# Optimization experiments

Hardware: AMD Instinct MI355X
Metric: run time of the kernel (lower is better)

## Reference

```python
import jax, jax.numpy as jnp
import numpy as np

B, H, W, C = 2, 128, 128, 256
D = 64          # attention_dim
NH = 1          # num_heads
P = 18          # num_random_points
N = H * W
EPS = 1e-5


def _layernorm(x, gamma, beta):
    mu = jnp.mean(x, axis=-1, keepdims=True)
    var = jnp.var(x, axis=-1, keepdims=True)
    return (x - mu) * jax.lax.rsqrt(var + EPS) * gamma + beta


def setup_inputs() -> dict:
    key = jax.random.key(0)
    ks = jax.random.split(key, 12)
    s = 0.02
    inp = {
        "X": jax.random.normal(ks[0], (B, H, W, C), dtype=jnp.float32),
        "selected_indices": jax.random.randint(ks[1], (B, N, P), 0, N),
        "topk": 1,
        "pos_enc": jax.random.normal(ks[2], (1, H, W, C), dtype=jnp.float32),
        "Wq": jax.random.normal(ks[3], (C, NH * D), dtype=jnp.float32) * s,
        "bq": jnp.zeros((NH * D,), dtype=jnp.float32),
        "Wk": jax.random.normal(ks[4], (C, NH * D), dtype=jnp.float32) * s,
        "bk": jnp.zeros((NH * D,), dtype=jnp.float32),
        "Wv": jax.random.normal(ks[5], (C, NH * D), dtype=jnp.float32) * s,
        "bv": jnp.zeros((NH * D,), dtype=jnp.float32),
        "Wo": jax.random.normal(ks[6], (NH * D, C), dtype=jnp.float32) * s,
        "bo": jnp.zeros((C,), dtype=jnp.float32),
        "W1": jax.random.normal(ks[7], (C, 4 * C), dtype=jnp.float32) * s,
        "b1": jnp.zeros((4 * C,), dtype=jnp.float32),
        "W2": jax.random.normal(ks[8], (4 * C, C), dtype=jnp.float32) * s,
        "b2": jnp.zeros((C,), dtype=jnp.float32),
        "g1": jnp.ones((C,), dtype=jnp.float32),
        "be1": jnp.zeros((C,), dtype=jnp.float32),
        "g2": jnp.ones((C,), dtype=jnp.float32),
        "be2": jnp.zeros((C,), dtype=jnp.float32),
    }
    return inp


def reference(X, selected_indices, topk, pos_enc, Wq, bq, Wk, bk, Wv, bv,
              Wo, bo, W1, b1, W2, b2, g1, be1, g2, be2):
    # forward_wotopk path (topk == 1)
    Xp = X + pos_enc                                  # [B,H,W,C]
    Q = (Xp @ Wq + bq).reshape(B, N, NH, D)
    K = (Xp @ Wk + bk).reshape(B, N, NH, D)
    V = (Xp @ Wv + bv).reshape(B, N, NH, D)

    # gather 18 random K/V rows per query pixel: [B,N,P,NH,D]
    gather = jax.vmap(lambda kv, idx: kv[idx])        # per-batch fancy index
    Ksel = gather(K, selected_indices)
    Vsel = gather(V, selected_indices)

    scores = jnp.einsum('bihd,bijhd->bijh', Q, Ksel) / jnp.sqrt(
        jnp.asarray(D, dtype=jnp.float32))
    attn = jax.nn.softmax(scores, axis=2)             # softmax over the P points
    ctx = jnp.einsum('bijh,bijhd->bihd', attn, Vsel).reshape(B, N, NH * D)

    out = (ctx @ Wo + bo).reshape(B, H, W, C)
    Xn = _layernorm(Xp + out, g1, be1)
    ffn = jax.nn.relu(Xn @ W1 + b1) @ W2 + b2
    out2 = _layernorm(Xn + ffn, g2, be2)
    return out2, attn
```

## Files before the change

kernel.cpp:

```cpp
#include <hip/hip_runtime.h>
#include <hip/hip_bf16.h>
#include <hip/hip_fp8.h>

#define CC 256
#define DD 64
#define PP 18
#define ROWS 32768
#define EPSF 1e-5f

typedef __attribute__((ext_vector_type(8))) short bf16x8;
typedef __attribute__((ext_vector_type(4))) short s16x4;
typedef __attribute__((ext_vector_type(4))) float f32x4;
typedef __attribute__((ext_vector_type(8))) int i32x8;

#define WAIT_VM(N) do {                                       \
    asm volatile("s_waitcnt vmcnt(" #N ")" ::: "memory");     \
    __builtin_amdgcn_s_barrier();                             \
    __builtin_amdgcn_sched_barrier(0);                        \
} while (0)

__device__ __forceinline__ void gl_lds16(const void* g, void* l) {
    __builtin_amdgcn_global_load_lds(
        (const __attribute__((address_space(1))) unsigned int*)g,
        (__attribute__((address_space(3))) unsigned int*)l, 16, 0, 0);
}

__device__ __forceinline__ void inv_swz128(int p, int& r, int& c) {
    r = p >> 7;
    c = ((p >> 4) & 7) ^ (r & 7);
}

__global__ __launch_bounds__(256) void k_prep(
    const float* __restrict__ Wq, const float* __restrict__ Wk,
    const float* __restrict__ Wv, const float* __restrict__ Wo,
    const float* __restrict__ W1, const float* __restrict__ W2,
    __hip_bfloat16* __restrict__ WqP, __hip_bfloat16* __restrict__ WkP,
    __hip_bfloat16* __restrict__ WvP, __hip_bfloat16* __restrict__ WoP,
    unsigned char* __restrict__ W1P8, __hip_bfloat16* __restrict__ W2T) {
    __shared__ float tile[32][33];
    const int b = blockIdx.x, t = threadIdx.x;
    if (b < 256) {
        int i = b * 256 + t;
        const float* src; __hip_bfloat16* dst; int K, N, j;
        if (i < 16384)      { src = Wq; dst = WqP; K = 256; N = 64;  j = i; }
        else if (i < 32768) { src = Wk; dst = WkP; K = 256; N = 64;  j = i - 16384; }
        else if (i < 49152) { src = Wv; dst = WvP; K = 256; N = 64;  j = i - 32768; }
        else                { src = Wo; dst = WoP; K = 64;  N = 256; j = i - 49152; }
        int e = j & 7, l = (j >> 3) & 63, rest = j >> 9;
        int KS = K >> 5;
        int ks = rest % KS, nt = rest / KS;
        int row = ks * 32 + (l >> 4) * 8 + e;
        int col = nt * 16 + (l & 15);
        dst[j] = __float2bfloat16(src[(long)row * N + col]);
        return;
    }
    if (b < 512) {
        int j0 = (b - 256) * 1024 + t * 4;
#pragma unroll
        for (int q = 0; q < 4; ++q) {
            int jj = j0 + q;
            int e = jj & 31, ll = (jj >> 5) & 63, rest = jj >> 11;
            int kb = rest & 1, nt = rest >> 1;
            int row = kb * 128 + (ll >> 4) * 32 + e;
            int col = nt * 16 + (ll & 15);
            __hip_fp8_e4m3 q8(W1[(long)row * 1024 + col]);
            W1P8[jj] = q8.__x;
        }
        return;
    }
    {
        int bb = b - 512;
        int r0 = (bb >> 3) * 32, c0 = (bb & 7) * 32;
#pragma unroll
        for (int i = 0; i < 4; ++i) {
            int idx = t + i * 256;
            int r = idx >> 5, c = idx & 31;
            tile[r][c] = W2[(long)(r0 + r) * 256 + c0 + c];
        }
        __syncthreads();
#pragma unroll
        for (int i = 0; i < 4; ++i) {
            int idx = t + i * 256;
            int c2 = idx >> 5, r2 = idx & 31;
            W2T[(long)(c0 + c2) * 1024 + r0 + r2] = __float2bfloat16(tile[r2][c2]);
        }
    }
}

__global__ __launch_bounds__(256) void k_qkv(
    const float4* __restrict__ X4, const float4* __restrict__ pe4,
    const __hip_bfloat16* __restrict__ WqP, const __hip_bfloat16* __restrict__ WkP,
    const __hip_bfloat16* __restrict__ WvP,
    const float* __restrict__ bq, const float* __restrict__ bk,
    const float* __restrict__ bv,
    __hip_bfloat16* __restrict__ Xpb,
    __hip_bfloat16* __restrict__ Qb, __hip_bfloat16* __restrict__ Kb,
    __hip_bfloat16* __restrict__ Vb) {
    __shared__ short Xs[32 * 256];
    const int t = threadIdx.x, w = t >> 6, l = t & 63;
    const int l15 = l & 15, lh = l >> 4;
    const int row0 = blockIdx.x * 32;

    for (int j = t; j < 2048; j += 256) {
        int r = j >> 6, c4 = j & 63;
        long g = row0 + r;
        float4 a = X4[(g << 6) + c4];
        float4 p = pe4[(long)((g & 16383) << 6) + c4];
        union { s16x4 v; __hip_bfloat16 h[4]; } u;
        u.h[0] = __float2bfloat16(a.x + p.x);
        u.h[1] = __float2bfloat16(a.y + p.y);
        u.h[2] = __float2bfloat16(a.z + p.z);
        u.h[3] = __float2bfloat16(a.w + p.w);
        int db = (r << 9) + (c4 << 3);
        db ^= (r & 7) << 4;
        *(s16x4*)((char*)Xs + db) = u.v;
        *(s16x4*)((char*)Xpb + (g << 9) + (c4 << 3)) = u.v;
    }
    __syncthreads();

    bf16x8 af[2][8];
#pragma unroll
    for (int ri = 0; ri < 2; ++ri)
#pragma unroll
        for (int ks = 0; ks < 8; ++ks) {
            int r = ri * 16 + l15;
            int db = (r << 9) + ks * 64 + lh * 16;
            db ^= (r & 7) << 4;
            af[ri][ks] = *(const bf16x8*)((const char*)Xs + db);
        }

    f32x4 acc[3][2];
#pragma unroll
    for (int j = 0; j < 3; ++j)
#pragma unroll
        for (int ri = 0; ri < 2; ++ri) acc[j][ri] = (f32x4)(0.f);

#pragma unroll
    for (int ks = 0; ks < 8; ++ks)
#pragma unroll
        for (int j = 0; j < 3; ++j) {
            int nt = w * 3 + j;
            const __hip_bfloat16* WP = (nt < 4) ? WqP : ((nt < 8) ? WkP : WvP);
            int ntl = nt & 3;
            bf16x8 b = *(const bf16x8*)(WP + (long)(((ntl * 8 + ks) << 6) + l) * 8);
#pragma unroll
            for (int ri = 0; ri < 2; ++ri)
                acc[j][ri] = __builtin_amdgcn_mfma_f32_16x16x32_bf16(
                    af[ri][ks], b, acc[j][ri], 0, 0, 0);
        }

#pragma unroll
    for (int j = 0; j < 3; ++j) {
        int nt = w * 3 + j;
        __hip_bfloat16* OP = (nt < 4) ? Qb : ((nt < 8) ? Kb : Vb);
        const float* BP = (nt < 4) ? bq : ((nt < 8) ? bk : bv);
        int col = (nt & 3) * 16 + l15;
        float bias = BP[col];
#pragma unroll
        for (int ri = 0; ri < 2; ++ri)
#pragma unroll
            for (int rg = 0; rg < 4; ++rg) {
                long row = row0 + ri * 16 + lh * 4 + rg;
                OP[row * DD + col] = __float2bfloat16(acc[j][ri][rg] + bias);
            }
    }
}

__global__ __launch_bounds__(256) void k_attn(const __hip_bfloat16* __restrict__ Q,
                                              const __hip_bfloat16* __restrict__ K,
                                              const __hip_bfloat16* __restrict__ V,
                                              const int* __restrict__ sel,
                                              __hip_bfloat16* __restrict__ ctx,
                                              float* __restrict__ attn_out) {
    const int wave  = threadIdx.x >> 6;
    const int lane  = threadIdx.x & 63;
    const int token = blockIdx.x * 4 + wave;
    const int b     = token >> 14;
    const int g = lane >> 3, s = lane & 7;

    const int* selp = sel + (long)token * PP;
    int sel_l = (lane < PP) ? selp[lane] : 0;

    float qf[8];
    {
        uint4 qv = *(const uint4*)(Q + (long)token * DD + s * 8);
        qf[0] = __uint_as_float(qv.x << 16);
        qf[1] = __uint_as_float(qv.x & 0xffff0000u);
        qf[2] = __uint_as_float(qv.y << 16);
        qf[3] = __uint_as_float(qv.y & 0xffff0000u);
        qf[4] = __uint_as_float(qv.z << 16);
        qf[5] = __uint_as_float(qv.z & 0xffff0000u);
        qf[6] = __uint_as_float(qv.w << 16);
        qf[7] = __uint_as_float(qv.w & 0xffff0000u);
    }

    const __hip_bfloat16* Kbase = K + (((long)b << 14) * DD);
    float sc[3];
    int idxs[3];
#pragma unroll
    for (int i = 0; i < 3; ++i) {
        int r = i * 8 + g;
        idxs[i] = __shfl(sel_l, r);
        uint4 kv = *(const uint4*)(Kbase + (long)idxs[i] * DD + s * 8);
        float part;
        part = qf[0] * __uint_as_float(kv.x << 16);
        part = fmaf(qf[1], __uint_as_float(kv.x & 0xffff0000u), part);
        part = fmaf(qf[2], __uint_as_float(kv.y << 16), part);
        part = fmaf(qf[3], __uint_as_float(kv.y & 0xffff0000u), part);
        part = fmaf(qf[4], __uint_as_float(kv.z << 16), part);
        part = fmaf(qf[5], __uint_as_float(kv.z & 0xffff0000u), part);
        part = fmaf(qf[6], __uint_as_float(kv.w << 16), part);
        part = fmaf(qf[7], __uint_as_float(kv.w & 0xffff0000u), part);
        part += __shfl_xor(part, 1);
        part += __shfl_xor(part, 2);
        part += __shfl_xor(part, 4);
        sc[i] = (r < PP) ? part * 0.125f : -1e30f;
    }

    float m = fmaxf(fmaxf(sc[0], sc[1]), sc[2]);
    m = fmaxf(m, __shfl_xor(m, 8));
    m = fmaxf(m, __shfl_xor(m, 16));
    m = fmaxf(m, __shfl_xor(m, 32));
    const float L2E = 1.4426950408889634f;
    float e0 = exp2f((sc[0] - m) * L2E);
    float e1 = exp2f((sc[1] - m) * L2E);
    float e2 = exp2f((sc[2] - m) * L2E);
    float dsum = e0 + e1 + e2;
    dsum += __shfl_xor(dsum, 8);
    dsum += __shfl_xor(dsum, 16);
    dsum += __shfl_xor(dsum, 32);
    float inv = 1.f / dsum;

    {
        int srcl = (lane & 7) << 3;
        float b0 = __shfl(e0, srcl);
        float b1 = __shfl(e1, srcl);
        float b2 = __shfl(e2, srcl);
        if (lane < PP) {
            float ev = (lane < 8) ? b0 : ((lane < 16) ? b1 : b2);
            attn_out[(long)token * PP + lane] = ev * inv;
        }
    }

    const __hip_bfloat16* Vbase = V + (((long)b << 14) * DD);
    float ca[8];
#pragma unroll
    for (int j = 0; j < 8; ++j) ca[j] = 0.f;
    float ev3[3] = {e0, e1, e2};
#pragma unroll
    for (int i = 0; i < 3; ++i) {
        uint4 vv = *(const uint4*)(Vbase + (long)idxs[i] * DD + s * 8);
        float e = ev3[i];
        ca[0] = fmaf(e, __uint_as_float(vv.x << 16), ca[0]);
        ca[1] = fmaf(e, __uint_as_float(vv.x & 0xffff0000u), ca[1]);
        ca[2] = fmaf(e, __uint_as_float(vv.y << 16), ca[2]);
        ca[3] = fmaf(e, __uint_as_float(vv.y & 0xffff0000u), ca[3]);
        ca[4] = fmaf(e, __uint_as_float(vv.z << 16), ca[4]);
        ca[5] = fmaf(e, __uint_as_float(vv.z & 0xffff0000u), ca[5]);
        ca[6] = fmaf(e, __uint_as_float(vv.w << 16), ca[6]);
        ca[7] = fmaf(e, __uint_as_float(vv.w & 0xffff0000u), ca[7]);
    }
#pragma unroll
    for (int o = 8; o <= 32; o <<= 1)
#pragma unroll
        for (int j = 0; j < 8; ++j) ca[j] += __shfl_xor(ca[j], o);
    if (g == 0) {
        union { bf16x8 v; __hip_bfloat16 h[8]; } u;
#pragma unroll
        for (int j = 0; j < 8; ++j) u.h[j] = __float2bfloat16(ca[j] * inv);
        *(bf16x8*)(ctx + (long)token * DD + s * 8) = u.v;
    }
}

__global__ __launch_bounds__(256) void k_projln(
    const __hip_bfloat16* __restrict__ ctx, const __hip_bfloat16* __restrict__ WoP,
    const float* __restrict__ bo, const float* __restrict__ g1,
    const float* __restrict__ be1,
    const __hip_bfloat16* __restrict__ Xpb, __hip_bfloat16* __restrict__ Xnb,
    unsigned char* __restrict__ Xn8) {
    __shared__ short Cs[32 * 64];
    __shared__ float red[2][32][2];
    __shared__ float mrs[32][2];
    const int t = threadIdx.x, w = t >> 6, l = t & 63;
    const int l15 = l & 15, lh = l >> 4;
    const int row0 = blockIdx.x * 32;

    {
        int r = t >> 3, ch = t & 7;
        int db = (r << 7) + (ch << 4);
        db ^= (r & 7) << 4;
        *(bf16x8*)((char*)Cs + db) = *(const bf16x8*)(ctx + (long)(row0 + r) * DD + ch * 8);
    }
    __syncthreads();

    const int ri = w & 1, nh = w >> 1;

    bf16x8 af[2];
#pragma unroll
    for (int ks = 0; ks < 2; ++ks) {
        int r = ri * 16 + l15;
        int db = (r << 7) + ks * 64 + lh * 16;
        db ^= (r & 7) << 4;
        af[ks] = *(const bf16x8*)((const char*)Cs + db);
    }

    f32x4 acc[8];
#pragma unroll
    for (int j = 0; j < 8; ++j) acc[j] = (f32x4)(0.f);

#pragma unroll
    for (int ks = 0; ks < 2; ++ks)
#pragma unroll
        for (int j = 0; j < 8; ++j) {
            int nt = nh * 8 + j;
            bf16x8 b = *(const bf16x8*)(WoP + (long)(((nt * 2 + ks) << 6) + l) * 8);
            acc[j] = __builtin_amdgcn_mfma_f32_16x16x32_bf16(af[ks], b, acc[j], 0, 0, 0);
        }

    float bov[8], g1v[8], be1v[8];
#pragma unroll
    for (int j = 0; j < 8; ++j) {
        int col = (nh * 8 + j) * 16 + l15;
        bov[j] = bo[col]; g1v[j] = g1[col]; be1v[j] = be1[col];
    }

    float xv[4][8];
#pragma unroll
    for (int rg = 0; rg < 4; ++rg) {
        long grow = row0 + ri * 16 + lh * 4 + rg;
        float s = 0.f, q = 0.f;
#pragma unroll
        for (int j = 0; j < 8; ++j) {
            float v = acc[j][rg] + bov[j] +
                      __bfloat162float(Xpb[grow * CC + (nh * 8 + j) * 16 + l15]);
            xv[rg][j] = v; s += v; q += v * v;
        }
#pragma unroll
        for (int o = 8; o > 0; o >>= 1) { s += __shfl_xor(s, o); q += __shfl_xor(q, o); }
        if (l15 == 0) {
            int rl = ri * 16 + lh * 4 + rg;
            red[nh][rl][0] = s; red[nh][rl][1] = q;
        }
    }
    __syncthreads();
    if (t < 32) {
        float S = red[0][t][0] + red[1][t][0];
        float Q = red[0][t][1] + red[1][t][1];
        float mu = S * (1.f / CC);
        float var = Q * (1.f / CC) - mu * mu;
        mrs[t][0] = mu; mrs[t][1] = rsqrtf(var + EPSF);
    }
    __syncthreads();
#pragma unroll
    for (int rg = 0; rg < 4; ++rg) {
        int rl = ri * 16 + lh * 4 + rg;
        long grow = row0 + rl;
        float mu = mrs[rl][0], rs = mrs[rl][1];
#pragma unroll
        for (int j = 0; j < 8; ++j) {
            int col = (nh * 8 + j) * 16 + l15;
            float vout = (xv[rg][j] - mu) * rs * g1v[j] + be1v[j];
            Xnb[grow * CC + col] = __float2bfloat16(vout);
            __hip_fp8_e4m3 q8(vout);
            Xn8[grow * CC + col] = q8.__x;
        }
    }
}

template<int GRL2, int CTL2>
__global__ __launch_bounds__(256) void k_gemm1mx(
    const unsigned char* __restrict__ X8,
    const unsigned char* __restrict__ W1P8,
    const float* __restrict__ bias,
    __hip_bfloat16* __restrict__ H) {
    __shared__ unsigned char Xs[128 * 256];

    const int t = threadIdx.x, w = t >> 6, l = t & 63;
    const int l15 = l & 15, lh = l >> 4;
    const int bid = blockIdx.x;
    const int wi = bid & ((1 << (GRL2 + CTL2)) - 1);
    const int rt = ((bid >> (GRL2 + CTL2)) << GRL2) | (wi & ((1 << GRL2) - 1));
    const int ct = wi >> GRL2;
    const int row0 = rt * 128, n0 = ct * 128;
    const int wr = w & 1, wc = w >> 1;

    for (int i = t; i < 2048; i += 256) {
        int r = i >> 4, c = i & 15;
        int pc = c ^ (r & 7);
        *(int4*)(Xs + r * 256 + pc * 16) =
            *(const int4*)(X8 + (long)(row0 + r) * 256 + c * 16);
    }
    __syncthreads();

    i32x8 afr[4][2];
#pragma unroll
    for (int f = 0; f < 4; ++f) {
        int row = wr * 64 + f * 16 + l15;
        int sw = row & 7;
#pragma unroll
        for (int kb = 0; kb < 2; ++kb) {
            int c0 = kb * 8 + lh * 2;
            int4 lo = *(const int4*)(Xs + row * 256 + (c0 ^ sw) * 16);
            int4 hi = *(const int4*)(Xs + row * 256 + ((c0 + 1) ^ sw) * 16);
            afr[f][kb][0] = lo.x; afr[f][kb][1] = lo.y;
            afr[f][kb][2] = lo.z; afr[f][kb][3] = lo.w;
            afr[f][kb][4] = hi.x; afr[f][kb][5] = hi.y;
            afr[f][kb][6] = hi.z; afr[f][kb][7] = hi.w;
        }
    }

    f32x4 acc[4][4];
#pragma unroll
    for (int i = 0; i < 4; ++i)
#pragma unroll
        for (int j = 0; j < 4; ++j) acc[i][j] = (f32x4)(0.f);

#pragma unroll
    for (int kb = 0; kb < 2; ++kb)
#pragma unroll
        for (int nf = 0; nf < 4; ++nf) {
            int nt = (n0 >> 4) + wc * 4 + nf;
            const unsigned char* bp = W1P8 + ((long)((nt * 2 + kb) * 64 + l)) * 32;
            int4 lo = *(const int4*)(bp);
            int4 hi = *(const int4*)(bp + 16);
            i32x8 bfr;
            bfr[0] = lo.x; bfr[1] = lo.y; bfr[2] = lo.z; bfr[3] = lo.w;
            bfr[4] = hi.x; bfr[5] = hi.y; bfr[6] = hi.z; bfr[7] = hi.w;
#pragma unroll
            for (int f = 0; f < 4; ++f)
                acc[f][nf] = __builtin_amdgcn_mfma_scale_f32_16x16x128_f8f6f4(
                    afr[f][kb], bfr, acc[f][nf], 0, 0, 0, 127, 0, 127);
        }

#pragma unroll
    for (int nf = 0; nf < 4; ++nf) {
        int col = n0 + wc * 64 + nf * 16 + l15;
        float bv = bias[col];
#pragma unroll
        for (int f = 0; f < 4; ++f)
#pragma unroll
            for (int rg = 0; rg < 4; ++rg) {
                int row = wr * 64 + f * 16 + lh * 4 + rg;
                long gi = (long)(row0 + row) * 1024 + col;
                H[gi] = __float2bfloat16(fmaxf(acc[f][nf][rg] + bv, 0.f));
            }
    }
}

__global__ __launch_bounds__(512) void k_gemm2ln(
    const __hip_bfloat16* __restrict__ A,
    const __hip_bfloat16* __restrict__ BT,
    const float* __restrict__ b2,
    const __hip_bfloat16* __restrict__ Res,
    const float* __restrict__ g2, const float* __restrict__ be2,
    float* __restrict__ out) {
    __shared__ short As[2][4096];
    __shared__ short Bs[2][16384];
    float* red = (float*)As;
    float* mrs = (float*)As + 512;

    const int t = threadIdx.x, w = t >> 6, l = t & 63;
    const int l15 = l & 15, lh = l >> 4;
    const int wr = w >> 2, wc = w & 3;
    const int row0 = blockIdx.x * 64;

    const __hip_bfloat16* gA;
    { int r, c; inv_swz128(t * 16, r, c); gA = A + (long)(row0 + r) * 1024 + c * 8; }
    const __hip_bfloat16* gB[4];
#pragma unroll
    for (int j = 0; j < 4; ++j) {
        int r, c;
        inv_swz128(j * 8192 + t * 16, r, c);
        gB[j] = BT + (long)r * 1024 + c * 8;
    }
    char* ldsA = (char*)As + w * 1024;
    char* ldsB = (char*)Bs + w * 1024;

    int offA[2][2], offB[4][2];
#pragma unroll
    for (int f = 0; f < 2; ++f) {
        int rowA = wr * 32 + f * 16 + l15;
        int sw = (rowA & 7) << 4;
#pragma unroll
        for (int kk = 0; kk < 2; ++kk)
            offA[f][kk] = rowA * 128 + ((kk * 64 + lh * 16) ^ sw);
    }
#pragma unroll
    for (int f = 0; f < 4; ++f) {
        int rowB = wc * 64 + f * 16 + l15;
        int sw = (rowB & 7) << 4;
#pragma unroll
        for (int kk = 0; kk < 2; ++kk)
            offB[f][kk] = rowB * 128 + ((kk * 64 + lh * 16) ^ sw);
    }

    f32x4 acc[2][4];
#pragma unroll
    for (int i = 0; i < 2; ++i)
#pragma unroll
        for (int j = 0; j < 4; ++j) acc[i][j] = (f32x4)(0.f);

#pragma unroll
    for (int n = 0; n < 2; ++n) {
        gl_lds16(gA + n * 64, ldsA + n * 8192);
#pragma unroll
        for (int j = 0; j < 4; ++j)
            gl_lds16(gB[j] + n * 64, ldsB + n * 32768 + j * 8192);
    }

#pragma unroll 1
    for (int ks = 0; ks < 16; ++ks) {
        if (ks + 1 < 16) { WAIT_VM(5); } else { WAIT_VM(0); }
        const char* as = (const char*)As + (ks & 1) * 8192;
        const char* bs = (const char*)Bs + (ks & 1) * 32768;
        bf16x8 afr[2][2], bfr[4][2];
#pragma unroll
        for (int f = 0; f < 2; ++f)
#pragma unroll
            for (int kk = 0; kk < 2; ++kk)
                afr[f][kk] = *(const bf16x8*)(as + offA[f][kk]);
#pragma unroll
        for (int f = 0; f < 4; ++f)
#pragma unroll
            for (int kk = 0; kk < 2; ++kk)
                bfr[f][kk] = *(const bf16x8*)(bs + offB[f][kk]);
        asm volatile("s_waitcnt lgkmcnt(0)" ::: "memory");
        __builtin_amdgcn_s_barrier();
        __builtin_amdgcn_sched_barrier(0);
        if (ks + 2 < 16) {
            gl_lds16(gA + (ks + 2) * 64, ldsA + (ks & 1) * 8192);
#pragma unroll
            for (int j = 0; j < 4; ++j)
                gl_lds16(gB[j] + (ks + 2) * 64, ldsB + (ks & 1) * 32768 + j * 8192);
        }
#pragma unroll
        for (int kk = 0; kk < 2; ++kk)
#pragma unroll
            for (int fr = 0; fr < 2; ++fr)
#pragma unroll
                for (int fc = 0; fc < 4; ++fc)
                    acc[fr][fc] = __builtin_amdgcn_mfma_f32_16x16x32_bf16(
                        afr[fr][kk], bfr[fc][kk], acc[fr][fc], 0, 0, 0);
    }

    float b2v[4], g2v[4], be2v[4];
#pragma unroll
    for (int fc = 0; fc < 4; ++fc) {
        int col = wc * 64 + fc * 16 + l15;
        b2v[fc] = b2[col]; g2v[fc] = g2[col]; be2v[fc] = be2[col];
    }
    __syncthreads();
#pragma unroll
    for (int fr = 0; fr < 2; ++fr)
#pragma unroll
        for (int rg = 0; rg < 4; ++rg) {
            int row = wr * 32 + fr * 16 + lh * 4 + rg;
            float s = 0.f, q = 0.f;
#pragma unroll
            for (int fc = 0; fc < 4; ++fc) {
                long gi = (long)(row0 + row) * CC + wc * 64 + fc * 16 + l15;
                float v = acc[fr][fc][rg] + b2v[fc] + __bfloat162float(Res[gi]);
                acc[fr][fc][rg] = v;
                s += v; q += v * v;
            }
#pragma unroll
            for (int o = 8; o > 0; o >>= 1) {
                s += __shfl_xor(s, o); q += __shfl_xor(q, o);
            }
            if (l15 == 0) {
                red[(wc * 64 + row) * 2 + 0] = s;
                red[(wc * 64 + row) * 2 + 1] = q;
            }
        }
    __syncthreads();
    if (t < 64) {
        float S = 0.f, Q = 0.f;
#pragma unroll
        for (int ww = 0; ww < 4; ++ww) {
            S += red[(ww * 64 + t) * 2 + 0];
            Q += red[(ww * 64 + t) * 2 + 1];
        }
        float mu = S * (1.f / CC);
        float var = Q * (1.f / CC) - mu * mu;
        mrs[t * 2 + 0] = mu; mrs[t * 2 + 1] = rsqrtf(var + EPSF);
    }
    __syncthreads();
#pragma unroll
    for (int fr = 0; fr < 2; ++fr)
#pragma unroll
        for (int rg = 0; rg < 4; ++rg) {
            int row = wr * 32 + fr * 16 + lh * 4 + rg;
            float mu = mrs[row * 2 + 0], rs = mrs[row * 2 + 1];
#pragma unroll
            for (int fc = 0; fc < 4; ++fc) {
                long gi = (long)(row0 + row) * CC + wc * 64 + fc * 16 + l15;
                out[gi] = (acc[fr][fc][rg] - mu) * rs * g2v[fc] + be2v[fc];
            }
        }
}

extern "C" void kernel_launch(void* const* d_in, const int* in_sizes, int n_in,
                              void* d_out, int out_size, void* d_ws, size_t ws_size,
                              hipStream_t stream) {
    const float* X   = (const float*)d_in[0];
    const int*   sel = (const int*)d_in[1];
    const float* pe  = (const float*)d_in[3];
    const float* Wq  = (const float*)d_in[4];
    const float* bq  = (const float*)d_in[5];
    const float* Wk  = (const float*)d_in[6];
    const float* bk  = (const float*)d_in[7];
    const float* Wv  = (const float*)d_in[8];
    const float* bv  = (const float*)d_in[9];
    const float* Wo  = (const float*)d_in[10];
    const float* bo  = (const float*)d_in[11];
    const float* W1  = (const float*)d_in[12];
    const float* b1  = (const float*)d_in[13];
    const float* W2  = (const float*)d_in[14];
    const float* b2  = (const float*)d_in[15];
    const float* g1  = (const float*)d_in[16];
    const float* be1 = (const float*)d_in[17];
    const float* g2  = (const float*)d_in[18];
    const float* be2 = (const float*)d_in[19];

    float* out = (float*)d_out;
    char*  ws  = (char*)d_ws;

    __hip_bfloat16* Xpb = (__hip_bfloat16*)(ws);
    __hip_bfloat16* Qb  = (__hip_bfloat16*)(ws + (16 << 20));
    __hip_bfloat16* Kb  = (__hip_bfloat16*)(ws + (20 << 20));
    __hip_bfloat16* Vb  = (__hip_bfloat16*)(ws + (24 << 20));
    __hip_bfloat16* ctxb= (__hip_bfloat16*)(ws + (28 << 20));
    __hip_bfloat16* H   = (__hip_bfloat16*)(ws + (16 << 20));
    unsigned char*  Xn8 = (unsigned char*)(ws + (88 << 20));
    __hip_bfloat16* WqP = (__hip_bfloat16*)(ws + (96 << 20));
    __hip_bfloat16* WkP = WqP + 16384;
    __hip_bfloat16* WvP = WkP + 16384;
    __hip_bfloat16* WoP = WvP + 16384;
    unsigned char*  W1P8= (unsigned char*)(WoP + 16384);
    __hip_bfloat16* W2T = (__hip_bfloat16*)(W1P8 + 262144);
    float* attn_out = out + (long)ROWS * CC;

    k_prep<<<768, 256, 0, stream>>>(Wq, Wk, Wv, Wo, W1, W2,
                                    WqP, WkP, WvP, WoP, W1P8, W2T);

    k_qkv<<<ROWS / 32, 256, 0, stream>>>((const float4*)X, (const float4*)pe,
                                         WqP, WkP, WvP, bq, bk, bv,
                                         Xpb, Qb, Kb, Vb);

    k_attn<<<ROWS / 4, 256, 0, stream>>>(Qb, Kb, Vb, sel, ctxb, attn_out);

    k_projln<<<ROWS / 32, 256, 0, stream>>>(ctxb, WoP, bo, g1, be1, Xpb, Xpb, Xn8);

    k_gemm1mx<2, 3><<<2048, 256, 0, stream>>>(Xn8, W1P8, b1, H);
    k_gemm2ln<<<512, 512, 0, stream>>>(H, W2T, b2, Xpb, g2, be2, out);
}
```

Baseline: 109.4 us.

## Quantize FFN hidden and W2 to FP8 and use MX MFMA for second GEMM

The FFN intermediate H is now written as FP8 e4m3 instead of bf16, and W2 is pre-packed into FP8 fragment layout. The second GEMM+LayerNorm kernel stages the whole 64x1024 FP8 row block into swizzled LDS once and uses scaled f8f6f4 MFMA, reading W2 fragments directly from global memory. This halves the H write/read traffic and doubles MFMA throughput, but drops the double-buffered async pipeline and adds FP8 quantization error on the hidden activations.

```diff
diff --git a/kernel.cpp b/kernel.cpp
--- a/kernel.cpp
+++ b/kernel.cpp
@@ -12,23 +12,6 @@
 typedef __attribute__((ext_vector_type(4))) short s16x4;
 typedef __attribute__((ext_vector_type(4))) float f32x4;
 typedef __attribute__((ext_vector_type(8))) int i32x8;
-
-#define WAIT_VM(N) do {                                       \
-    asm volatile("s_waitcnt vmcnt(" #N ")" ::: "memory");     \
-    __builtin_amdgcn_s_barrier();                             \
-    __builtin_amdgcn_sched_barrier(0);                        \
-} while (0)
-
-__device__ __forceinline__ void gl_lds16(const void* g, void* l) {
-    __builtin_amdgcn_global_load_lds(
-        (const __attribute__((address_space(1))) unsigned int*)g,
-        (__attribute__((address_space(3))) unsigned int*)l, 16, 0, 0);
-}
-
-__device__ __forceinline__ void inv_swz128(int p, int& r, int& c) {
-    r = p >> 7;
-    c = ((p >> 4) & 7) ^ (r & 7);
-}
 
 __global__ __launch_bounds__(256) void k_prep(
     const float* __restrict__ Wq, const float* __restrict__ Wk,
@@ -36,8 +19,7 @@
     const float* __restrict__ W1, const float* __restrict__ W2,
     __hip_bfloat16* __restrict__ WqP, __hip_bfloat16* __restrict__ WkP,
     __hip_bfloat16* __restrict__ WvP, __hip_bfloat16* __restrict__ WoP,
-    unsigned char* __restrict__ W1P8, __hip_bfloat16* __restrict__ W2T) {
-    __shared__ float tile[32][33];
+    unsigned char* __restrict__ W1P8, unsigned char* __restrict__ W2P8) {
     const int b = blockIdx.x, t = threadIdx.x;
     if (b < 256) {
         int i = b * 256 + t;
@@ -69,20 +51,16 @@
         return;
     }
     {
-        int bb = b - 512;
-        int r0 = (bb >> 3) * 32, c0 = (bb & 7) * 32;
-#pragma unroll
-        for (int i = 0; i < 4; ++i) {
-            int idx = t + i * 256;
-            int r = idx >> 5, c = idx & 31;
-            tile[r][c] = W2[(long)(r0 + r) * 256 + c0 + c];
-        }
-        __syncthreads();
-#pragma unroll
-        for (int i = 0; i < 4; ++i) {
-            int idx = t + i * 256;
-            int c2 = idx >> 5, r2 = idx & 31;
-            W2T[(long)(c0 + c2) * 1024 + r0 + r2] = __float2bfloat16(tile[r2][c2]);
+        int j0 = (b - 512) * 1024 + t * 4;
+#pragma unroll
+        for (int q = 0; q < 4; ++q) {
+            int jj = j0 + q;
+            int e = jj & 31, ll = (jj >> 5) & 63, rest = jj >> 11;
+            int kb = rest & 7, nt = rest >> 3;
+            int row = kb * 128 + (ll >> 4) * 32 + e;
+            int col = nt * 16 + (ll & 15);
+            __hip_fp8_e4m3 q8(W2[(long)row * 256 + col]);
+            W2P8[jj] = q8.__x;
         }
     }
 }
@@ -372,7 +350,7 @@
     const unsigned char* __restrict__ X8,
     const unsigned char* __restrict__ W1P8,
     const float* __restrict__ bias,
-    __hip_bfloat16* __restrict__ H) {
+    unsigned char* __restrict__ H8) {
     __shared__ unsigned char Xs[128 * 256];
 
     const int t = threadIdx.x, w = t >> 6, l = t & 63;
@@ -442,57 +420,39 @@
             for (int rg = 0; rg < 4; ++rg) {
                 int row = wr * 64 + f * 16 + lh * 4 + rg;
                 long gi = (long)(row0 + row) * 1024 + col;
-                H[gi] = __float2bfloat16(fmaxf(acc[f][nf][rg] + bv, 0.f));
+                __hip_fp8_e4m3 q8(fmaxf(acc[f][nf][rg] + bv, 0.f));
+                H8[gi] = q8.__x;
             }
     }
 }
 
-__global__ __launch_bounds__(512) void k_gemm2ln(
-    const __hip_bfloat16* __restrict__ A,
-    const __hip_bfloat16* __restrict__ BT,
+__global__ __launch_bounds__(512) void k_gemm2lnmx(
+    const unsigned char* __restrict__ H8,
+    const unsigned char* __restrict__ W2P8,
     const float* __restrict__ b2,
     const __hip_bfloat16* __restrict__ Res,
     const float* __restrict__ g2, const float* __restrict__ be2,
     float* __restrict__ out) {
-    __shared__ short As[2][4096];
-    __shared__ short Bs[2][16384];
-    float* red = (float*)As;
-    float* mrs = (float*)As + 512;
+    __shared__ unsigned char Hs[64 * 1024];
+    __shared__ float red[4][64][2];
+    __shared__ float mrs[64][2];
 
     const int t = threadIdx.x, w = t >> 6, l = t & 63;
     const int l15 = l & 15, lh = l >> 4;
     const int wr = w >> 2, wc = w & 3;
     const int row0 = blockIdx.x * 64;
 
-    const __hip_bfloat16* gA;
-    { int r, c; inv_swz128(t * 16, r, c); gA = A + (long)(row0 + r) * 1024 + c * 8; }
-    const __hip_bfloat16* gB[4];
-#pragma unroll
-    for (int j = 0; j < 4; ++j) {
-        int r, c;
-        inv_swz128(j * 8192 + t * 16, r, c);
-        gB[j] = BT + (long)r * 1024 + c * 8;
-    }
-    char* ldsA = (char*)As + w * 1024;
-    char* ldsB = (char*)Bs + w * 1024;
-
-    int offA[2][2], offB[4][2];
-#pragma unroll
-    for (int f = 0; f < 2; ++f) {
-        int rowA = wr * 32 + f * 16 + l15;
-        int sw = (rowA & 7) << 4;
-#pragma unroll
-        for (int kk = 0; kk < 2; ++kk)
-            offA[f][kk] = rowA * 128 + ((kk * 64 + lh * 16) ^ sw);
-    }
-#pragma unroll
-    for (int f = 0; f < 4; ++f) {
-        int rowB = wc * 64 + f * 16 + l15;
-        int sw = (rowB & 7) << 4;
-#pragma unroll
-        for (int kk = 0; kk < 2; ++kk)
-            offB[f][kk] = rowB * 128 + ((kk * 64 + lh * 16) ^ sw);
-    }
+    {
+        int r = t >> 3, sw = r & 7;
+        const unsigned char* src = H8 + (long)(row0 + r) * 1024;
+        unsigned char* dst = Hs + r * 1024;
+#pragma unroll
+        for (int j = 0; j < 8; ++j) {
+            int c = (t & 7) + j * 8;
+            *(int4*)(dst + (c ^ sw) * 16) = *(const int4*)(src + c * 16);
+        }
+    }
+    __syncthreads();
 
     f32x4 acc[2][4];
 #pragma unroll
@@ -500,47 +460,34 @@
 #pragma unroll
         for (int j = 0; j < 4; ++j) acc[i][j] = (f32x4)(0.f);
 
-#pragma unroll
-    for (int n = 0; n < 2; ++n) {
-        gl_lds16(gA + n * 64, ldsA + n * 8192);
-#pragma unroll
-        for (int j = 0; j < 4; ++j)
-            gl_lds16(gB[j] + n * 64, ldsB + n * 32768 + j * 8192);
-    }
-
-#pragma unroll 1
-    for (int ks = 0; ks < 16; ++ks) {
-        if (ks + 1 < 16) { WAIT_VM(5); } else { WAIT_VM(0); }
-        const char* as = (const char*)As + (ks & 1) * 8192;
-        const char* bs = (const char*)Bs + (ks & 1) * 32768;
-        bf16x8 afr[2][2], bfr[4][2];
-#pragma unroll
-        for (int f = 0; f < 2; ++f)
-#pragma unroll
-            for (int kk = 0; kk < 2; ++kk)
-                afr[f][kk] = *(const bf16x8*)(as + offA[f][kk]);
-#pragma unroll
-        for (int f = 0; f < 4; ++f)
-#pragma unroll
-            for (int kk = 0; kk < 2; ++kk)
-                bfr[f][kk] = *(const bf16x8*)(bs + offB[f][kk]);
-        asm volatile("s_waitcnt lgkmcnt(0)" ::: "memory");
-        __builtin_amdgcn_s_barrier();
-        __builtin_amdgcn_sched_barrier(0);
-        if (ks + 2 < 16) {
-            gl_lds16(gA + (ks + 2) * 64, ldsA + (ks & 1) * 8192);
-#pragma unroll
-            for (int j = 0; j < 4; ++j)
-                gl_lds16(gB[j] + (ks + 2) * 64, ldsB + (ks & 1) * 32768 + j * 8192);
-        }
-#pragma unroll
-        for (int kk = 0; kk < 2; ++kk)
-#pragma unroll
-            for (int fr = 0; fr < 2; ++fr)
-#pragma unroll
-                for (int fc = 0; fc < 4; ++fc)
-                    acc[fr][fc] = __builtin_amdgcn_mfma_f32_16x16x32_bf16(
-                        afr[fr][kk], bfr[fc][kk], acc[fr][fc], 0, 0, 0);
+#pragma unroll 2
+    for (int kb = 0; kb < 8; ++kb) {
+        i32x8 afr[2];
+#pragma unroll
+        for (int f = 0; f < 2; ++f) {
+            int row = wr * 32 + f * 16 + l15;
+            int sw = row & 7;
+            int c0 = kb * 8 + lh * 2;
+            const unsigned char* hp = Hs + row * 1024;
+            int4 lo = *(const int4*)(hp + ((c0 ^ sw) << 4));
+            int4 hi = *(const int4*)(hp + (((c0 + 1) ^ sw) << 4));
+            afr[f][0] = lo.x; afr[f][1] = lo.y; afr[f][2] = lo.z; afr[f][3] = lo.w;
+            afr[f][4] = hi.x; afr[f][5] = hi.y; afr[f][6] = hi.z; afr[f][7] = hi.w;
+        }
+#pragma unroll
+        for (int nf = 0; nf < 4; ++nf) {
+            int nt = wc * 4 + nf;
+            const unsigned char* bp = W2P8 + ((long)((nt * 8 + kb) * 64 + l)) * 32;
+            int4 lo = *(const int4*)(bp);
+            int4 hi = *(const int4*)(bp + 16);
+            i32x8 bfr;
+            bfr[0] = lo.x; bfr[1] = lo.y; bfr[2] = lo.z; bfr[3] = lo.w;
+            bfr[4] = hi.x; bfr[5] = hi.y; bfr[6] = hi.z; bfr[7] = hi.w;
+#pragma unroll
+            for (int f = 0; f < 2; ++f)
+                acc[f][nf] = __builtin_amdgcn_mfma_scale_f32_16x16x128_f8f6f4(
+                    afr[f], bfr, acc[f][nf], 0, 0, 0, 127, 0, 127);
+        }
     }
 
     float b2v[4], g2v[4], be2v[4];
@@ -549,7 +496,6 @@
         int col = wc * 64 + fc * 16 + l15;
         b2v[fc] = b2[col]; g2v[fc] = g2[col]; be2v[fc] = be2[col];
     }
-    __syncthreads();
 #pragma unroll
     for (int fr = 0; fr < 2; ++fr)
 #pragma unroll
@@ -567,22 +513,16 @@
             for (int o = 8; o > 0; o >>= 1) {
                 s += __shfl_xor(s, o); q += __shfl_xor(q, o);
             }
-            if (l15 == 0) {
-                red[(wc * 64 + row) * 2 + 0] = s;
-                red[(wc * 64 + row) * 2 + 1] = q;
-            }
+            if (l15 == 0) { red[wc][row][0] = s; red[wc][row][1] = q; }
         }
     __syncthreads();
     if (t < 64) {
         float S = 0.f, Q = 0.f;
 #pragma unroll
-        for (int ww = 0; ww < 4; ++ww) {
-            S += red[(ww * 64 + t) * 2 + 0];
-            Q += red[(ww * 64 + t) * 2 + 1];
-        }
+        for (int ww = 0; ww < 4; ++ww) { S += red[ww][t][0]; Q += red[ww][t][1]; }
         float mu = S * (1.f / CC);
         float var = Q * (1.f / CC) - mu * mu;
-        mrs[t * 2 + 0] = mu; mrs[t * 2 + 1] = rsqrtf(var + EPSF);
+        mrs[t][0] = mu; mrs[t][1] = rsqrtf(var + EPSF);
     }
     __syncthreads();
 #pragma unroll
@@ -590,7 +530,7 @@
 #pragma unroll
         for (int rg = 0; rg < 4; ++rg) {
             int row = wr * 32 + fr * 16 + lh * 4 + rg;
-            float mu = mrs[row * 2 + 0], rs = mrs[row * 2 + 1];
+            float mu = mrs[row][0], rs = mrs[row][1];
 #pragma unroll
             for (int fc = 0; fc < 4; ++fc) {
                 long gi = (long)(row0 + row) * CC + wc * 64 + fc * 16 + l15;
@@ -630,18 +570,18 @@
     __hip_bfloat16* Kb  = (__hip_bfloat16*)(ws + (20 << 20));
     __hip_bfloat16* Vb  = (__hip_bfloat16*)(ws + (24 << 20));
     __hip_bfloat16* ctxb= (__hip_bfloat16*)(ws + (28 << 20));
-    __hip_bfloat16* H   = (__hip_bfloat16*)(ws + (16 << 20));
+    unsigned char*  H8  = (unsigned char*)(ws + (40 << 20));
     unsigned char*  Xn8 = (unsigned char*)(ws + (88 << 20));
     __hip_bfloat16* WqP = (__hip_bfloat16*)(ws + (96 << 20));
     __hip_bfloat16* WkP = WqP + 16384;
     __hip_bfloat16* WvP = WkP + 16384;
     __hip_bfloat16* WoP = WvP + 16384;
     unsigned char*  W1P8= (unsigned char*)(WoP + 16384);
-    __hip_bfloat16* W2T = (__hip_bfloat16*)(W1P8 + 262144);
+    unsigned char*  W2P8= W1P8 + 262144;
     float* attn_out = out + (long)ROWS * CC;
 
     k_prep<<<768, 256, 0, stream>>>(Wq, Wk, Wv, Wo, W1, W2,
-                                    WqP, WkP, WvP, WoP, W1P8, W2T);
+                                    WqP, WkP, WvP, WoP, W1P8, W2P8);
 
     k_qkv<<<ROWS / 32, 256, 0, stream>>>((const float4*)X, (const float4*)pe,
                                          WqP, WkP, WvP, bq, bk, bv,
@@ -651,6 +591,6 @@
 
     k_projln<<<ROWS / 32, 256, 0, stream>>>(ctxb, WoP, bo, g1, be1, Xpb, Xpb, Xn8);
 
-    k_gemm1mx<2, 3><<<2048, 256, 0, stream>>>(Xn8, W1P8, b1, H);
-    k_gemm2ln<<<512, 512, 0, stream>>>(H, W2T, b2, Xpb, g2, be2, out);
-}
+    k_gemm1mx<2, 3><<<2048, 256, 0, stream>>>(Xn8, W1P8, b1, H8);
+    k_gemm2lnmx<<<512, 512, 0, stream>>>(H8, W2P8, b2, Xpb, g2, be2, out);
+}
```

After: 111.6 us. 1.02x slower.
